# Optimization experiments

Hardware: AMD Instinct MI355X
Metric: run time of the kernel (lower is better)

## Reference

```python
import math
import jax, jax.numpy as jnp
import numpy as np

H, PQ, PV, E, C, S, N = 12, 4, 8, 16, 128, 384, 512


def setup_inputs() -> dict:
    key = jax.random.key(0)
    ks = jax.random.split(key, 16)
    rn = lambda k, shape, scale=1.0: jax.random.normal(k, shape, jnp.float32) * scale
    single = rn(ks[0], (N, S))
    pair = rn(ks[1], (N, N, C))
    R, _ = jnp.linalg.qr(rn(ks[2], (N, 3, 3)))  # proper orthonormal frames
    t = rn(ks[3], (N, 3))
    w = 0.02
    return dict(
        single_representation=single,
        pair_representation=pair,
        rotations=R,
        translations=t,
        Wq=rn(ks[4], (H, S, E), w),
        Wk=rn(ks[5], (H, S, E), w),
        Wv=rn(ks[6], (H, S, E), w),
        Wqp=rn(ks[7], (H, PQ, S, 3), w),
        Wkp=rn(ks[8], (H, PQ, S, 3), w),
        Wvp=rn(ks[9], (H, PV, S, 3), w),
        Wb=rn(ks[10], (H, C), w),
        Wout=rn(ks[11], (H * (C + E + PV * 4), S), w),
        b_out=jnp.zeros((S,), jnp.float32),
        scale_head=jnp.ones((H,), jnp.float32),
    )


def _frame_apply(R, t, pts):
    # R:[N,3,3], t:[N,3], pts:[H,P,N,3] -> R_n @ p + t_n per residue n
    return jnp.einsum('nij,hpnj->hpni', R, pts) + t[None, None, :, :]


def reference(single_representation, pair_representation, rotations, translations,
              Wq, Wk, Wv, Wqp, Wkp, Wvp, Wb, Wout, b_out, scale_head):
    single, pair = single_representation, pair_representation
    n = single.shape[0]

    # --- sequence QK term ---
    q = jnp.einsum('nd,hde->hne', single, Wq)
    k = jnp.einsum('nd,hde->hne', single, Wk)
    w_single = math.sqrt(1.0 / E) * jnp.einsum('hne,hme->hnm', q, k)  # [H,N,N]

    # --- pair bias term ---
    w_pair = jnp.einsum('nmc,hc->hnm', pair, Wb)  # [H,N,N]

    # --- frame (3D point distance) term ---
    qp = jnp.einsum('nd,hpdk->hpnk', single, Wqp)  # [H,PQ,N,3]
    kp = jnp.einsum('nd,hpdk->hpnk', single, Wkp)
    lqp = _frame_apply(rotations, translations, qp)
    lkp = _frame_apply(rotations, translations, kp)
    diff = lqp[:, :, :, None, :] - lkp[:, :, None, :, :]   # [H,PQ,N,N,3]
    sqd = jnp.sum(diff * diff, axis=(1, 4))                 # [H,N,N] (sum over points & xyz)
    w_frame = (-math.sqrt(1.0 / (18 * PQ))) * jax.nn.softplus(scale_head)[:, None, None] * sqd

    w = jax.nn.softmax(w_single + w_pair + w_frame, axis=-1)  # [H,N,N]

    # --- sequence value aggregation ---
    v = jnp.einsum('nd,hde->hne', single, Wv)
    att_single = jnp.einsum('hnm,hme->hne', w, v)             # [H,N,E]
    att_single = jnp.transpose(att_single, (1, 0, 2)).reshape(n, -1)

    # --- pair value aggregation (faithful to source: sums over query index too) ---
    colsum = jnp.sum(w, axis=1)                               # [H,N] = sum_a w[h,a,b]
    att_pair = jnp.einsum('hb,ibc->hic', colsum, pair)        # [H,N,C]
    att_pair = jnp.transpose(att_pair, (1, 0, 2)).reshape(n, -1)

    # --- 3D point value aggregation ---
    vp = jnp.einsum('nd,hpdk->hpnk', single, Wvp)             # [H,PV,N,3]
    lvp = _frame_apply(rotations, translations, vp)
    local_out = jnp.einsum('hnm,hpmk->hpnk', w, lvp)          # [H,PV,N,3]
    Rinv = jnp.swapaxes(rotations, -1, -2)                    # R^T
    tinv = -jnp.einsum('nij,nj->ni', Rinv, translations)      # -R^T t
    global_out = _frame_apply(Rinv, tinv, local_out)          # [H,PV,N,3]
    out_points = jnp.transpose(global_out, (2, 1, 0, 3)).reshape(n, -1)  # [N, PV*H*3]
    out_norm = jnp.linalg.norm(global_out, axis=-1)           # [H,PV,N]
    out_norm = jnp.transpose(out_norm, (2, 1, 0)).reshape(n, -1)         # [N, PV*H]

    att = jnp.concatenate([att_single, att_pair, out_points, out_norm], axis=-1)
    return att @ Wout + b_out
```

## Files before the change

### kernel.cpp

```cpp
#include <hip/hip_runtime.h>
#include <math.h>

#define NRES 512
#define HH 12
#define PQn 4
#define PVn 8
#define En 16
#define Cn 128
#define Sn 384
#define ATT_COLS 2112

#define OFF_Q    0
#define OFF_K    (OFF_Q   + HH*NRES*En)
#define OFF_V    (OFF_K   + HH*NRES*En)
#define OFF_LQP  (OFF_V   + HH*NRES*En)
#define OFF_LKP  (OFF_LQP + HH*NRES*12)
#define OFF_LVP  (OFF_LKP + HH*NRES*12)
#define OFF_CS   (OFF_LVP + HH*NRES*24)
#define OFF_ATT  (OFF_CS  + NRES*HH)
#define OFF_LG   (OFF_ATT + NRES*ATT_COLS)
#define OFF_PART OFF_LG
#define OFF_KC   OFF_ATT
#define OFF_D1   (OFF_KC + NRES*HH*28)
#define OFF_D0   (OFF_D1 + NRES*HH)
#define OFF_QC   (OFF_D0 + NRES*HH)
#define KSPLIT 16
#define KCHUNK (ATT_COLS/KSPLIT)
#define OROWS 8

__global__ __launch_bounds__(256) void ipa_proj(
    const float* __restrict__ single, const float* __restrict__ Rm,
    const float* __restrict__ tr,
    const float* __restrict__ Wq, const float* __restrict__ Wk,
    const float* __restrict__ Wv, const float* __restrict__ Wqp,
    const float* __restrict__ Wkp, const float* __restrict__ Wvp,
    float* __restrict__ ws)
{
  float* q   = ws + OFF_Q;  float* k   = ws + OFF_K;  float* v   = ws + OFF_V;
  float* lqp = ws + OFF_LQP; float* lkp = ws + OFF_LKP; float* lvp = ws + OFF_LVP;
  const int n0 = blockIdx.x * 8;
  const int g  = blockIdx.y;
  const int tid = threadIdx.x;
  __shared__ float sS[8][388];
  __shared__ float sR[8][9];
  __shared__ float sT[8][3];
  #pragma unroll
  for (int i = 0; i < 3; ++i) {
    int idx = i*256 + tid;
    int r = idx / 96, c4 = idx % 96;
    float4 val = *reinterpret_cast<const float4*>(single + (size_t)(n0 + r)*Sn + c4*4);
    *reinterpret_cast<float4*>(&sS[r][c4*4]) = val;
  }
  if (tid < 72)      sR[tid/9][tid%9] = Rm[(size_t)(n0 + tid/9)*9 + tid%9];
  else if (tid < 96) { int r = (tid-72)/3; sT[r][(tid-72)%3] = tr[(size_t)(n0+r)*3 + (tid-72)%3]; }
  __syncthreads();
  #pragma unroll
  for (int i = 0; i < 3; ++i) {
    int item = i*256 + tid;
    int nl = item & 7;
    int ul = item >> 3;
    int u  = g*96 + ul;
    const float* srow = sS[nl];
    if (u < 576) {
      int which = u/192, r = u%192, h = r>>4, e = r&15;
      const float* W = (which==0 ? Wq : which==1 ? Wk : Wv) + (size_t)h*Sn*En + e;
      float acc = 0.f;
      #pragma unroll 8
      for (int d = 0; d < Sn; ++d) acc = fmaf(srow[d], W[(size_t)d*En], acc);
      float* dst = (which==0 ? q : which==1 ? k : v);
      dst[((size_t)h*NRES + (n0+nl))*En + e] = acc;
    } else {
      int u2 = u - 576;
      const float* W; float* dst;
      if (u2 < 48)      { int h=u2>>2,     p=u2&3;      W = Wqp + (size_t)(h*PQn+p)*Sn*3; dst = lqp + ((size_t)h*NRES + (n0+nl))*12 + p*3; }
      else if (u2 < 96) { int h=(u2-48)>>2,p=(u2-48)&3; W = Wkp + (size_t)(h*PQn+p)*Sn*3; dst = lkp + ((size_t)h*NRES + (n0+nl))*12 + p*3; }
      else              { int h=(u2-96)>>3,p=(u2-96)&7; W = Wvp + (size_t)(h*PVn+p)*Sn*3; dst = lvp + ((size_t)h*NRES + (n0+nl))*24 + p*3; }
      float x0=0.f,x1=0.f,x2=0.f;
      #pragma unroll 4
      for (int d = 0; d < Sn; ++d) {
        float sv = srow[d];
        x0 = fmaf(sv, W[d*3+0], x0);
        x1 = fmaf(sv, W[d*3+1], x1);
        x2 = fmaf(sv, W[d*3+2], x2);
      }
      const float* R8 = sR[nl]; const float* T8 = sT[nl];
      dst[0] = R8[0]*x0 + R8[1]*x1 + R8[2]*x2 + T8[0];
      dst[1] = R8[3]*x0 + R8[4]*x1 + R8[5]*x2 + T8[1];
      dst[2] = R8[6]*x0 + R8[7]*x1 + R8[8]*x2 + T8[2];
    }
  }
}

__global__ __launch_bounds__(256) void ipa_pack(
    const float* __restrict__ scale_head, float* __restrict__ ws)
{
  const float* q   = ws + OFF_Q;
  const float* k   = ws + OFF_K;
  const float* lkp = ws + OFF_LKP;
  const float* lqp = ws + OFF_LQP;
  float* kc = ws + OFF_KC;
  float* qc = ws + OFF_QC;
  float* d1 = ws + OFF_D1;
  float* d0 = ws + OFF_D0;
  const int idx = blockIdx.x*256 + threadIdx.x;
  const int h = idx >> 9, m = idx & 511;
  const float gamma = 0.11785113019775793f * log1pf(__expf(scale_head[h]));
  const float* kr  = k   + ((size_t)h*NRES + m)*En;
  const float* qr  = q   + ((size_t)h*NRES + m)*En;
  const float* lkr = lkp + ((size_t)h*NRES + m)*12;
  const float* lqr = lqp + ((size_t)h*NRES + m)*12;
  float* kcr = kc + ((size_t)m*HH + h)*28;
  float* qcr = qc + ((size_t)m*HH + h)*28;
  #pragma unroll
  for (int e = 0; e < En; ++e) { kcr[e] = 0.25f * kr[e]; qcr[e] = qr[e]; }
  float Bm = 0.f, An = 0.f;
  #pragma unroll
  for (int j = 0; j < 12; ++j) {
    float b = lkr[j], a = lqr[j];
    kcr[16+j] = (2.f*gamma)*b;
    qcr[16+j] = a;
    Bm = fmaf(b, b, Bm);
    An = fmaf(a, a, An);
  }
  d1[m*HH + h] = -gamma*Bm;
  d0[m*HH + h] = -gamma*An;
}

__global__ __launch_bounds__(256, 3) void ipa_logits(
    const float* __restrict__ pair, const float* __restrict__ Wb,
    float* __restrict__ ws)
{
  const float* kc = ws + OFF_KC;
  const float* qc = ws + OFF_QC;
  const float* d1 = ws + OFF_D1;
  const float* d0 = ws + OFF_D0;
  float* lg = ws + OFF_LG;
  const int n = blockIdx.x;
  const int m = blockIdx.y * 256 + threadIdx.x;

  float4 row[32];
  const float4* prow = reinterpret_cast<const float4*>(pair + ((size_t)n*NRES + m)*Cn);
  #pragma unroll
  for (int j = 0; j < 32; ++j) row[j] = prow[j];

  float d1v[HH];
  {
    const float4* dd = reinterpret_cast<const float4*>(d1 + (size_t)m*HH);
    float4 a = dd[0], b = dd[1], c = dd[2];
    d1v[0]=a.x; d1v[1]=a.y; d1v[2]=a.z; d1v[3]=a.w;
    d1v[4]=b.x; d1v[5]=b.y; d1v[6]=b.z; d1v[7]=b.w;
    d1v[8]=c.x; d1v[9]=c.y; d1v[10]=c.z; d1v[11]=c.w;
  }
  const float* kcrow = kc + (size_t)m*HH*28;
  const float* qcrow = qc + (size_t)n*HH*28;
  const float* d0row = d0 + (size_t)n*HH;

  #pragma unroll
  for (int h = 0; h < HH; ++h) {
    const float4* kcr = reinterpret_cast<const float4*>(kcrow + h*28);
    const float4* qcr = reinterpret_cast<const float4*>(qcrow + h*28);
    const float4* wbr = reinterpret_cast<const float4*>(Wb + h*Cn);
    float s = d1v[h] + d0row[h];
    #pragma unroll
    for (int c4 = 0; c4 < 32; ++c4) {
      float4 p = row[c4];
      float4 w = wbr[c4];
      s += p.x*w.x + p.y*w.y + p.z*w.z + p.w*w.w;
    }
    #pragma unroll
    for (int j = 0; j < 7; ++j) {
      float4 kv = kcr[j];
      float4 qv = qcr[j];
      s += kv.x*qv.x + kv.y*qv.y + kv.z*qv.z + kv.w*qv.w;
    }
    lg[((size_t)h*NRES + n)*NRES + m] = s;
  }
}

__global__ __launch_bounds__(256) void ipa_softmax(float* __restrict__ ws)
{
  float* lg = ws + OFF_LG;
  const int row  = blockIdx.x*4 + (threadIdx.x >> 6);
  const int lane = threadIdx.x & 63;
  float4* p = reinterpret_cast<float4*>(lg + (size_t)row*NRES);
  float4 x0 = p[lane];
  float4 x1 = p[64 + lane];
  float mx = fmaxf(fmaxf(fmaxf(x0.x,x0.y),fmaxf(x0.z,x0.w)),
                   fmaxf(fmaxf(x1.x,x1.y),fmaxf(x1.z,x1.w)));
  #pragma unroll
  for (int off = 32; off >= 1; off >>= 1) mx = fmaxf(mx, __shfl_xor(mx, off));
  x0.x = __expf(x0.x-mx); x0.y = __expf(x0.y-mx); x0.z = __expf(x0.z-mx); x0.w = __expf(x0.w-mx);
  x1.x = __expf(x1.x-mx); x1.y = __expf(x1.y-mx); x1.z = __expf(x1.z-mx); x1.w = __expf(x1.w-mx);
  float sum = x0.x+x0.y+x0.z+x0.w + x1.x+x1.y+x1.z+x1.w;
  #pragma unroll
  for (int off = 32; off >= 1; off >>= 1) sum += __shfl_xor(sum, off);
  const float inv = 1.f/sum;
  x0.x*=inv; x0.y*=inv; x0.z*=inv; x0.w*=inv;
  x1.x*=inv; x1.y*=inv; x1.z*=inv; x1.w*=inv;
  p[lane] = x0;
  p[64 + lane] = x1;
}

__global__ __launch_bounds__(256) void ipa_colsum(float* __restrict__ ws)
{
  const float* lg = ws + OFF_LG;
  float* cs = ws + OFF_CS;
  const int h = blockIdx.x, ac = blockIdx.y, tid = threadIdx.x;
  const float* base = lg + (size_t)h*NRES*NRES + (size_t)ac*64*NRES;
  float acc0 = 0.f, acc1 = 0.f;
  #pragma unroll 4
  for (int a = 0; a < 64; ++a) {
    acc0 += base[(size_t)a*NRES + tid];
    acc1 += base[(size_t)a*NRES + tid + 256];
  }
  atomicAdd(&cs[(size_t)tid*HH + h],       acc0);
  atomicAdd(&cs[(size_t)(tid+256)*HH + h], acc1);
}

__global__ __launch_bounds__(256) void ipa_agg(
    const float* __restrict__ Rm, const float* __restrict__ tr,
    float* __restrict__ ws)
{
  const float* v   = ws + OFF_V;
  const float* lvp = ws + OFF_LVP;
  const float* lg  = ws + OFF_LG;
  float* att = ws + OFF_ATT;
  const int row  = blockIdx.x*4 + (threadIdx.x >> 6);
  const int lane = threadIdx.x & 63;
  const int h = row >> 9, n = row & 511;

  float acc[40];
  #pragma unroll
  for (int i = 0; i < 40; ++i) acc[i] = 0.f;

  const float* wrow = lg + (size_t)row*NRES;
  #pragma unroll 2
  for (int j = 0; j < 8; ++j) {
    const int m = j*64 + lane;
    const float wv = wrow[m];
    const float4* v4 = reinterpret_cast<const float4*>(v + ((size_t)h*NRES + m)*En);
    float4 a0=v4[0], a1=v4[1], a2=v4[2], a3=v4[3];
    acc[0]+=wv*a0.x; acc[1]+=wv*a0.y; acc[2]+=wv*a0.z; acc[3]+=wv*a0.w;
    acc[4]+=wv*a1.x; acc[5]+=wv*a1.y; acc[6]+=wv*a1.z; acc[7]+=wv*a1.w;
    acc[8]+=wv*a2.x; acc[9]+=wv*a2.y; acc[10]+=wv*a2.z; acc[11]+=wv*a2.w;
    acc[12]+=wv*a3.x; acc[13]+=wv*a3.y; acc[14]+=wv*a3.z; acc[15]+=wv*a3.w;
    const float4* l4 = reinterpret_cast<const float4*>(lvp + ((size_t)h*NRES + m)*24);
    #pragma unroll
    for (int t = 0; t < 6; ++t) {
      float4 b = l4[t];
      acc[16+4*t+0]+=wv*b.x; acc[16+4*t+1]+=wv*b.y;
      acc[16+4*t+2]+=wv*b.z; acc[16+4*t+3]+=wv*b.w;
    }
  }
  #pragma unroll
  for (int off = 32; off >= 1; off >>= 1) {
    #pragma unroll
    for (int i = 0; i < 40; ++i) acc[i] += __shfl_xor(acc[i], off);
  }
  if (lane == 0) {
    size_t ab = (size_t)n*ATT_COLS;
    float4* as = reinterpret_cast<float4*>(att + ab + h*En);
    as[0] = make_float4(acc[0],acc[1],acc[2],acc[3]);
    as[1] = make_float4(acc[4],acc[5],acc[6],acc[7]);
    as[2] = make_float4(acc[8],acc[9],acc[10],acc[11]);
    as[3] = make_float4(acc[12],acc[13],acc[14],acc[15]);
    const float R0=Rm[n*9+0],R1=Rm[n*9+1],R2=Rm[n*9+2],
                R3=Rm[n*9+3],R4=Rm[n*9+4],R5=Rm[n*9+5],
                R6=Rm[n*9+6],R7=Rm[n*9+7],R8=Rm[n*9+8];
    const float t0=tr[n*3+0], t1=tr[n*3+1], t2=tr[n*3+2];
    #pragma unroll
    for (int pp = 0; pp < 8; ++pp) {
      float d0 = acc[16+3*pp+0]-t0, d1 = acc[16+3*pp+1]-t1, d2 = acc[16+3*pp+2]-t2;
      float g0 = R0*d0 + R3*d1 + R6*d2;
      float g1 = R1*d0 + R4*d1 + R7*d2;
      float g2 = R2*d0 + R5*d1 + R8*d2;
      att[ab + 1728 + (pp*HH + h)*3 + 0] = g0;
      att[ab + 1728 + (pp*HH + h)*3 + 1] = g1;
      att[ab + 1728 + (pp*HH + h)*3 + 2] = g2;
      att[ab + 2016 + pp*HH + h] = sqrtf(g0*g0 + g1*g1 + g2*g2);
    }
  }
}

__global__ __launch_bounds__(256) void ipa_pairagg(
    const float* __restrict__ pair, float* __restrict__ ws)
{
  const float* cs = ws + OFF_CS;
  float* att = ws + OFF_ATT;
  const int i = blockIdx.x, tid = threadIdx.x;
  __shared__ float sCS[NRES*HH];
  __shared__ float4 sRed[4][HH][32];
  #pragma unroll
  for (int it = 0; it < 6; ++it) {
    int idx = it*256 + tid;
    reinterpret_cast<float4*>(sCS)[idx] = reinterpret_cast<const float4*>(cs)[idx];
  }
  __syncthreads();
  const int c4 = tid & 31, bg = tid >> 5;
  const int b0 = bg * 64;
  float4 acc[HH];
  #pragma unroll
  for (int h = 0; h < HH; ++h) acc[h] = make_float4(0.f,0.f,0.f,0.f);
  const float* prow = pair + (size_t)i*NRES*Cn;
  for (int jb = 0; jb < 64; jb += 4) {
    float4 pv[4];
    #pragma unroll
    for (int u = 0; u < 4; ++u)
      pv[u] = *reinterpret_cast<const float4*>(prow + (size_t)(b0+jb+u)*Cn + c4*4);
    #pragma unroll
    for (int u = 0; u < 4; ++u) {
      const float4* csr = reinterpret_cast<const float4*>(&sCS[(b0+jb+u)*HH]);
      float4 c0 = csr[0], c1 = csr[1], c2 = csr[2];
      float w[12] = {c0.x,c0.y,c0.z,c0.w, c1.x,c1.y,c1.z,c1.w, c2.x,c2.y,c2.z,c2.w};
      #pragma unroll
      for (int h = 0; h < HH; ++h) {
        acc[h].x = fmaf(w[h], pv[u].x, acc[h].x);
        acc[h].y = fmaf(w[h], pv[u].y, acc[h].y);
        acc[h].z = fmaf(w[h], pv[u].z, acc[h].z);
        acc[h].w = fmaf(w[h], pv[u].w, acc[h].w);
      }
    }
  }
  if (bg >= 4) {
    for (int h = 0; h < HH; ++h) sRed[bg-4][h][c4] = acc[h];
  }
  __syncthreads();
  if (bg < 4) {
    for (int h = 0; h < HH; ++h) {
      float4 b2 = sRed[bg][h][c4];
      acc[h].x+=b2.x; acc[h].y+=b2.y; acc[h].z+=b2.z; acc[h].w+=b2.w;
    }
  }
  __syncthreads();
  if (bg >= 2 && bg < 4) {
    for (int h = 0; h < HH; ++h) sRed[bg-2][h][c4] = acc[h];
  }
  __syncthreads();
  if (bg < 2) {
    for (int h = 0; h < HH; ++h) {
      float4 b2 = sRed[bg][h][c4];
      acc[h].x+=b2.x; acc[h].y+=b2.y; acc[h].z+=b2.z; acc[h].w+=b2.w;
    }
  }
  __syncthreads();
  if (bg == 1) {
    for (int h = 0; h < HH; ++h) sRed[0][h][c4] = acc[h];
  }
  __syncthreads();
  if (bg == 0) {
    size_t base = (size_t)i*ATT_COLS + 192;
    for (int h = 0; h < HH; ++h) {
      float4 b2 = sRed[0][h][c4];
      acc[h].x+=b2.x; acc[h].y+=b2.y; acc[h].z+=b2.z; acc[h].w+=b2.w;
      *reinterpret_cast<float4*>(att + base + h*Cn + c4*4) = acc[h];
    }
  }
}

__global__ __launch_bounds__(384) void ipa_outp(
    const float* __restrict__ att, const float* __restrict__ Wout,
    float* __restrict__ ws)
{
  float* partial = ws + OFF_PART;
  const int rb = blockIdx.x;
  const int ks = blockIdx.y;
  const int s  = threadIdx.x;
  const int n0 = rb*OROWS;
  const int j0 = ks*KCHUNK;

  float acc[OROWS];
  #pragma unroll
  for (int r = 0; r < OROWS; ++r) acc[r] = 0.f;

  for (int jg = 0; jg < KCHUNK/4; ++jg) {
    const int j = j0 + jg*4;
    float w0 = Wout[(size_t)(j+0)*Sn + s];
    float w1 = Wout[(size_t)(j+1)*Sn + s];
    float w2 = Wout[(size_t)(j+2)*Sn + s];
    float w3 = Wout[(size_t)(j+3)*Sn + s];
    #pragma unroll
    for (int r = 0; r < OROWS; ++r) {
      float4 av = *reinterpret_cast<const float4*>(att + (size_t)(n0+r)*ATT_COLS + j);
      acc[r] = fmaf(av.x, w0, acc[r]);
      acc[r] = fmaf(av.y, w1, acc[r]);
      acc[r] = fmaf(av.z, w2, acc[r]);
      acc[r] = fmaf(av.w, w3, acc[r]);
    }
  }
  #pragma unroll
  for (int r = 0; r < OROWS; ++r)
    partial[((size_t)ks*NRES + n0 + r)*Sn + s] = acc[r];
}

__global__ __launch_bounds__(384) void ipa_outred(
    const float* __restrict__ b_out, float* __restrict__ ws,
    float* __restrict__ out)
{
  const float* partial = ws + OFF_PART;
  const int n = blockIdx.x, s = threadIdx.x;
  float a = b_out[s];
  #pragma unroll
  for (int ks = 0; ks < KSPLIT; ++ks)
    a += partial[((size_t)ks*NRES + n)*Sn + s];
  out[(size_t)n*Sn + s] = a;
}

extern "C" void kernel_launch(void* const* d_in, const int* in_sizes, int n_in,
                              void* d_out, int out_size, void* d_ws, size_t ws_size,
                              hipStream_t stream) {
  const float* single = (const float*)d_in[0];
  const float* pair   = (const float*)d_in[1];
  const float* Rm     = (const float*)d_in[2];
  const float* tr     = (const float*)d_in[3];
  const float* Wq     = (const float*)d_in[4];
  const float* Wk     = (const float*)d_in[5];
  const float* Wv     = (const float*)d_in[6];
  const float* Wqp    = (const float*)d_in[7];
  const float* Wkp    = (const float*)d_in[8];
  const float* Wvp    = (const float*)d_in[9];
  const float* Wb     = (const float*)d_in[10];
  const float* Wout   = (const float*)d_in[11];
  const float* b_out  = (const float*)d_in[12];
  const float* scale_head = (const float*)d_in[13];
  float* ws  = (float*)d_ws;
  float* out = (float*)d_out;

  hipMemsetAsync(ws + OFF_CS, 0, NRES*HH*sizeof(float), stream);
  ipa_proj   <<<dim3(64, 8),  256, 0, stream>>>(single, Rm, tr, Wq, Wk, Wv, Wqp, Wkp, Wvp, ws);
  ipa_pack   <<<dim3(24),     256, 0, stream>>>(scale_head, ws);
  ipa_logits <<<dim3(NRES, 2), 256, 0, stream>>>(pair, Wb, ws);
  ipa_softmax<<<dim3(HH*NRES/4), 256, 0, stream>>>(ws);
  ipa_colsum <<<dim3(HH, 8),  256, 0, stream>>>(ws);
  ipa_agg    <<<dim3(HH*NRES/4), 256, 0, stream>>>(Rm, tr, ws);
  ipa_pairagg<<<dim3(NRES),   256, 0, stream>>>(pair, ws);
  ipa_outp   <<<dim3(NRES/OROWS, KSPLIT), 384, 0, stream>>>(ws + OFF_ATT, Wout, ws);
  ipa_outred <<<dim3(NRES),   384, 0, stream>>>(b_out, ws, out);
}
```

Measured before the change: 281.9 us.

## Coalesce pair reads in logits kernel and widen colsum/pairagg parallelism

Rewrites the logits kernel so four lanes cooperate on one pair row, reading it in coalesced 16-byte chunks with nontemporal loads. Wb is staged in shared memory, and partial dot products are combined with lane shuffles, each lane then finishing three heads. The colsum grid is doubled, and pairagg moves to 512 threads with an extra reduction stage and nontemporal pair loads. The aim is better memory coalescing and occupancy on the pair tensor streams, at the cost of shuffle overhead and more atomics.

Result: slower. 335.6 us (+19.0%).

```diff
diff --git a/kernel.cpp b/kernel.cpp
--- a/kernel.cpp
+++ b/kernel.cpp
@@ -9,6 +9,8 @@
 #define Cn 128
 #define Sn 384
 #define ATT_COLS 2112
+
+typedef float f4 __attribute__((ext_vector_type(4)));
 
 #define OFF_Q    0
 #define OFF_K    (OFF_Q   + HH*NRES*En)
@@ -126,7 +128,7 @@
   d0[m*HH + h] = -gamma*An;
 }
 
-__global__ __launch_bounds__(256, 3) void ipa_logits(
+__global__ __launch_bounds__(256, 4) void ipa_logits(
     const float* __restrict__ pair, const float* __restrict__ Wb,
     float* __restrict__ ws)
 {
@@ -135,45 +137,81 @@
   const float* d1 = ws + OFF_D1;
   const float* d0 = ws + OFF_D0;
   float* lg = ws + OFF_LG;
-  const int n = blockIdx.x;
-  const int m = blockIdx.y * 256 + threadIdx.x;
-
-  float4 row[32];
-  const float4* prow = reinterpret_cast<const float4*>(pair + ((size_t)n*NRES + m)*Cn);
-  #pragma unroll
-  for (int j = 0; j < 32; ++j) row[j] = prow[j];
-
-  float d1v[HH];
-  {
-    const float4* dd = reinterpret_cast<const float4*>(d1 + (size_t)m*HH);
-    float4 a = dd[0], b = dd[1], c = dd[2];
-    d1v[0]=a.x; d1v[1]=a.y; d1v[2]=a.z; d1v[3]=a.w;
-    d1v[4]=b.x; d1v[5]=b.y; d1v[6]=b.z; d1v[7]=b.w;
-    d1v[8]=c.x; d1v[9]=c.y; d1v[10]=c.z; d1v[11]=c.w;
-  }
-  const float* kcrow = kc + (size_t)m*HH*28;
-  const float* qcrow = qc + (size_t)n*HH*28;
-  const float* d0row = d0 + (size_t)n*HH;
-
+
+  __shared__ float sWb[HH*Cn];
+  for (int i = threadIdx.x; i < HH*Cn/4; i += 256)
+    reinterpret_cast<float4*>(sWb)[i] = reinterpret_cast<const float4*>(Wb)[i];
+  __syncthreads();
+
+  const int n    = blockIdx.x;
+  const int tid  = threadIdx.x;
+  const int lane = tid & 63;
+  const int wave = tid >> 6;
+  const int r    = lane >> 2;
+  const int cq   = lane & 3;
+  const int m    = blockIdx.y*128 + wave*16 + r;
+  const int m2   = m + 64;
+
+  const float* p1 = pair + ((size_t)n*NRES + m )*Cn + cq*4;
+  const float* p2 = pair + ((size_t)n*NRES + m2)*Cn + cq*4;
+  f4 pv[8], pw[8];
+  #pragma unroll
+  for (int jg = 0; jg < 8; ++jg) {
+    pv[jg] = __builtin_nontemporal_load(reinterpret_cast<const f4*>(p1 + jg*16));
+    pw[jg] = __builtin_nontemporal_load(reinterpret_cast<const f4*>(p2 + jg*16));
+  }
+
+  float acc1[HH], acc2[HH];
+  #pragma unroll
+  for (int h = 0; h < HH; ++h) { acc1[h] = 0.f; acc2[h] = 0.f; }
+  #pragma unroll
+  for (int jg = 0; jg < 8; ++jg) {
+    #pragma unroll
+    for (int h = 0; h < HH; ++h) {
+      const float4 wb = *reinterpret_cast<const float4*>(&sWb[h*Cn + jg*16 + cq*4]);
+      acc1[h] += pv[jg].x*wb.x + pv[jg].y*wb.y + pv[jg].z*wb.z + pv[jg].w*wb.w;
+      acc2[h] += pw[jg].x*wb.x + pw[jg].y*wb.y + pw[jg].z*wb.z + pw[jg].w*wb.w;
+    }
+  }
   #pragma unroll
   for (int h = 0; h < HH; ++h) {
-    const float4* kcr = reinterpret_cast<const float4*>(kcrow + h*28);
-    const float4* qcr = reinterpret_cast<const float4*>(qcrow + h*28);
-    const float4* wbr = reinterpret_cast<const float4*>(Wb + h*Cn);
-    float s = d1v[h] + d0row[h];
-    #pragma unroll
-    for (int c4 = 0; c4 < 32; ++c4) {
-      float4 p = row[c4];
-      float4 w = wbr[c4];
-      s += p.x*w.x + p.y*w.y + p.z*w.z + p.w*w.w;
-    }
+    acc1[h] += __shfl_xor(acc1[h], 1);
+    acc1[h] += __shfl_xor(acc1[h], 2);
+    acc2[h] += __shfl_xor(acc2[h], 1);
+    acc2[h] += __shfl_xor(acc2[h], 2);
+  }
+  float b10, b11, b12, b20, b21, b22;
+  if      (cq == 0) { b10=acc1[0]; b11=acc1[1];  b12=acc1[2];
+                      b20=acc2[0]; b21=acc2[1];  b22=acc2[2]; }
+  else if (cq == 1) { b10=acc1[3]; b11=acc1[4];  b12=acc1[5];
+                      b20=acc2[3]; b21=acc2[4];  b22=acc2[5]; }
+  else if (cq == 2) { b10=acc1[6]; b11=acc1[7];  b12=acc1[8];
+                      b20=acc2[6]; b21=acc2[7];  b22=acc2[8]; }
+  else              { b10=acc1[9]; b11=acc1[10]; b12=acc1[11];
+                      b20=acc2[9]; b21=acc2[10]; b22=acc2[11]; }
+
+  const int hb = 3*cq;
+  const float* kc1 = kc + ((size_t)m *HH + hb)*28;
+  const float* kc2 = kc + ((size_t)m2*HH + hb)*28;
+  const float* qcn = qc + ((size_t)n *HH + hb)*28;
+  const float* d0n = d0 + (size_t)n*HH + hb;
+  const float* d11 = d1 + (size_t)m *HH + hb;
+  const float* d12 = d1 + (size_t)m2*HH + hb;
+
+  #pragma unroll
+  for (int i = 0; i < 3; ++i) {
+    float t1 = (i==0 ? b10 : i==1 ? b11 : b12) + d11[i] + d0n[i];
+    float t2 = (i==0 ? b20 : i==1 ? b21 : b22) + d12[i] + d0n[i];
     #pragma unroll
     for (int j = 0; j < 7; ++j) {
-      float4 kv = kcr[j];
-      float4 qv = qcr[j];
-      s += kv.x*qv.x + kv.y*qv.y + kv.z*qv.z + kv.w*qv.w;
-    }
-    lg[((size_t)h*NRES + n)*NRES + m] = s;
+      float4 qv = *reinterpret_cast<const float4*>(qcn + i*28 + j*4);
+      float4 k1 = *reinterpret_cast<const float4*>(kc1 + i*28 + j*4);
+      float4 k2 = *reinterpret_cast<const float4*>(kc2 + i*28 + j*4);
+      t1 += k1.x*qv.x + k1.y*qv.y + k1.z*qv.z + k1.w*qv.w;
+      t2 += k2.x*qv.x + k2.y*qv.y + k2.z*qv.z + k2.w*qv.w;
+    }
+    lg[((size_t)(hb+i)*NRES + n)*NRES + m ] = t1;
+    lg[((size_t)(hb+i)*NRES + n)*NRES + m2] = t2;
   }
 }
 
@@ -206,12 +244,12 @@
   const float* lg = ws + OFF_LG;
   float* cs = ws + OFF_CS;
   const int h = blockIdx.x, ac = blockIdx.y, tid = threadIdx.x;
-  const float* base = lg + (size_t)h*NRES*NRES + (size_t)ac*64*NRES;
+  const float* base = lg + (size_t)h*NRES*NRES + (size_t)ac*32*NRES;
   float acc0 = 0.f, acc1 = 0.f;
   #pragma unroll 4
-  for (int a = 0; a < 64; ++a) {
-    acc0 += base[(size_t)a*NRES + tid];
-    acc1 += base[(size_t)a*NRES + tid + 256];
+  for (int a = 0; a < 32; ++a) {
+    acc0 += __builtin_nontemporal_load(&base[(size_t)a*NRES + tid]);
+    acc1 += __builtin_nontemporal_load(&base[(size_t)a*NRES + tid + 256]);
   }
   atomicAdd(&cs[(size_t)tid*HH + h],       acc0);
   atomicAdd(&cs[(size_t)(tid+256)*HH + h], acc1);
@@ -282,31 +320,29 @@
   }
 }
 
-__global__ __launch_bounds__(256) void ipa_pairagg(
+__global__ __launch_bounds__(512) void ipa_pairagg(
     const float* __restrict__ pair, float* __restrict__ ws)
 {
   const float* cs = ws + OFF_CS;
   float* att = ws + OFF_ATT;
   const int i = blockIdx.x, tid = threadIdx.x;
   __shared__ float sCS[NRES*HH];
-  __shared__ float4 sRed[4][HH][32];
-  #pragma unroll
-  for (int it = 0; it < 6; ++it) {
-    int idx = it*256 + tid;
+  __shared__ float4 sRed[8][HH][32];
+  for (int idx = tid; idx < NRES*HH/4; idx += 512)
     reinterpret_cast<float4*>(sCS)[idx] = reinterpret_cast<const float4*>(cs)[idx];
-  }
   __syncthreads();
   const int c4 = tid & 31, bg = tid >> 5;
-  const int b0 = bg * 64;
+  const int b0 = bg * 32;
   float4 acc[HH];
   #pragma unroll
   for (int h = 0; h < HH; ++h) acc[h] = make_float4(0.f,0.f,0.f,0.f);
   const float* prow = pair + (size_t)i*NRES*Cn;
-  for (int jb = 0; jb < 64; jb += 4) {
-    float4 pv[4];
+  for (int jb = 0; jb < 32; jb += 4) {
+    f4 pv[4];
     #pragma unroll
     for (int u = 0; u < 4; ++u)
-      pv[u] = *reinterpret_cast<const float4*>(prow + (size_t)(b0+jb+u)*Cn + c4*4);
+      pv[u] = __builtin_nontemporal_load(
+          reinterpret_cast<const f4*>(prow + (size_t)(b0+jb+u)*Cn + c4*4));
     #pragma unroll
     for (int u = 0; u < 4; ++u) {
       const float4* csr = reinterpret_cast<const float4*>(&sCS[(b0+jb+u)*HH]);
@@ -321,7 +357,18 @@
       }
     }
   }
-  if (bg >= 4) {
+  if (bg >= 8) {
+    for (int h = 0; h < HH; ++h) sRed[bg-8][h][c4] = acc[h];
+  }
+  __syncthreads();
+  if (bg < 8) {
+    for (int h = 0; h < HH; ++h) {
+      float4 b2 = sRed[bg][h][c4];
+      acc[h].x+=b2.x; acc[h].y+=b2.y; acc[h].z+=b2.z; acc[h].w+=b2.w;
+    }
+  }
+  __syncthreads();
+  if (bg >= 4 && bg < 8) {
     for (int h = 0; h < HH; ++h) sRed[bg-4][h][c4] = acc[h];
   }
   __syncthreads();
@@ -428,11 +475,11 @@
   hipMemsetAsync(ws + OFF_CS, 0, NRES*HH*sizeof(float), stream);
   ipa_proj   <<<dim3(64, 8),  256, 0, stream>>>(single, Rm, tr, Wq, Wk, Wv, Wqp, Wkp, Wvp, ws);
   ipa_pack   <<<dim3(24),     256, 0, stream>>>(scale_head, ws);
-  ipa_logits <<<dim3(NRES, 2), 256, 0, stream>>>(pair, Wb, ws);
+  ipa_logits <<<dim3(NRES, 4), 256, 0, stream>>>(pair, Wb, ws);
   ipa_softmax<<<dim3(HH*NRES/4), 256, 0, stream>>>(ws);
-  ipa_colsum <<<dim3(HH, 8),  256, 0, stream>>>(ws);
+  ipa_colsum <<<dim3(HH, 16), 256, 0, stream>>>(ws);
   ipa_agg    <<<dim3(HH*NRES/4), 256, 0, stream>>>(Rm, tr, ws);
-  ipa_pairagg<<<dim3(NRES),   256, 0, stream>>>(pair, ws);
+  ipa_pairagg<<<dim3(NRES),   512, 0, stream>>>(pair, ws);
   ipa_outp   <<<dim3(NRES/OROWS, KSPLIT), 384, 0, stream>>>(ws + OFF_ATT, Wout, ws);
   ipa_outred <<<dim3(NRES),   384, 0, stream>>>(b_out, ws, out);
 }
```
